# Kernel optimization log

Measured on AMD Instinct MI355X. Metric: run time of the kernel, lower is better.

Reference implementation:

```python
import jax, jax.numpy as jnp
import numpy as np

NHEAD = 16

def setup_inputs() -> dict:
    key = jax.random.key(0)
    ks = jax.random.split(key, 5)
    B, S, D = 4, 2048, 1024
    x = jax.random.normal(ks[0], (B, S, D), dtype=jnp.float32)
    in_proj_weight = jax.random.normal(ks[1], (3 * D, D), dtype=jnp.float32) * (D ** -0.5)
    in_proj_bias = jax.random.normal(ks[2], (3 * D,), dtype=jnp.float32) * 0.02
    out_w = jax.random.normal(ks[3], (D, D), dtype=jnp.float32) * (D ** -0.5)
    out_b = jax.random.normal(ks[4], (D,), dtype=jnp.float32) * 0.02
    return {"x": x, "in_proj_weight": in_proj_weight, "in_proj_bias": in_proj_bias,
            "out_w": out_w, "out_b": out_b}

def reference(x, in_proj_weight, in_proj_bias, out_w, out_b):
    # Faithful to nn.MultiheadAttention self-attn (prefill path, no mask).
    B, S, D = x.shape
    H = NHEAD
    hd = D // H
    qkv = x @ in_proj_weight.T + in_proj_bias            # [B,S,3D]
    q, k, v = jnp.split(qkv, 3, axis=-1)                 # each [B,S,D]
    def heads(t):
        return t.reshape(B, S, H, hd).transpose(0, 2, 1, 3)  # [B,H,S,hd]
    q, k, v = heads(q), heads(k), heads(v)
    scale = hd ** -0.5
    scores = jnp.einsum('bhqd,bhkd->bhqk', q * scale, k)  # [B,H,S,S]
    attn = jax.nn.softmax(scores, axis=-1)
    o = jnp.einsum('bhqk,bhkd->bhqd', attn, v)            # [B,H,S,hd]
    o = o.transpose(0, 2, 1, 3).reshape(B, S, D)
    return o @ out_w.T + out_b
```

## Files before the change

### kernel.cpp

```cpp
#include <hip/hip_runtime.h>
#include <hip/hip_bf16.h>
#include <math.h>

typedef __bf16 bf16_t;
typedef __bf16 bf16x8 __attribute__((ext_vector_type(8)));
typedef float  f32x4  __attribute__((ext_vector_type(4)));

#define DEV __device__ __forceinline__

#define BSZ    4
#define SEQ    2048
#define DMODEL 1024
#define NHEADS 16
#define HDIM   64
#define MROWS  (BSZ*SEQ)
#define KDIM   1024
#define NQKV   (3*DMODEL)

#define GLOAD_LDS16(src, dst)                                                  \
  __builtin_amdgcn_global_load_lds(                                            \
      (__attribute__((address_space(1))) void*)(void*)(src),                   \
      (__attribute__((address_space(3))) void*)(dst), 16, 0, 0)

DEV unsigned cvtpk_bf16(float lo, float hi) {
  unsigned r;
  asm("v_cvt_pk_bf16_f32 %0, %1, %2" : "=v"(r) : "v"(lo), "v"(hi));
  return r;
}

__global__ void cast3_f32_to_bf16(const float* __restrict__ a, int na4,
                                  const float* __restrict__ b, int nb4,
                                  const float* __restrict__ c, int nc4,
                                  bf16_t* __restrict__ oa,
                                  bf16_t* __restrict__ ob,
                                  bf16_t* __restrict__ oc) {
  union U { bf16_t h[4]; uint2 u; };
  int total = na4 + nb4 + nc4;
  for (int i = blockIdx.x * blockDim.x + threadIdx.x; i < total;
       i += gridDim.x * blockDim.x) {
    const float* src; bf16_t* dst; int k;
    if (i < na4)            { src = a; dst = oa; k = i; }
    else if (i < na4 + nb4) { src = b; dst = ob; k = i - na4; }
    else                    { src = c; dst = oc; k = i - na4 - nb4; }
    float4 v = reinterpret_cast<const float4*>(src)[k];
    U r;
    r.h[0] = (bf16_t)v.x; r.h[1] = (bf16_t)v.y;
    r.h[2] = (bf16_t)v.z; r.h[3] = (bf16_t)v.w;
    reinterpret_cast<uint2*>(dst)[k] = r.u;
  }
}

DEV void gemm_tile(const bf16_t* __restrict__ A, const bf16_t* __restrict__ Bt,
                   int row0, int col0, char* smem, f32x4 acc[4][4]) {
  const int t    = threadIdx.x;
  const int lane = t & 63;
  const int wid  = t >> 6;
  const int wm   = (wid >> 1) * 64;
  const int wn   = (wid & 1) * 64;
  const int l15  = lane & 15;
  const int lhi  = lane >> 4;

  char* As = smem;
  char* Bs = smem + 16384;

  const f32x4 fzero = {0.f, 0.f, 0.f, 0.f};
#pragma unroll
  for (int mi = 0; mi < 4; mi++)
#pragma unroll
    for (int ni = 0; ni < 4; ni++) acc[mi][ni] = fzero;

  const char* Abase = (const char*)A;
  const char* Bbase = (const char*)Bt;

  for (int k0 = 0; k0 < KDIM; k0 += 64) {
    __syncthreads();
#pragma unroll
    for (int i = 0; i < 4; i++) {
      int o   = (t + i * 256) * 16;
      int row = o >> 7;
      int cbs = (o & 127) ^ ((row & 7) << 4);
      GLOAD_LDS16(Abase + ((size_t)(row0 + row) * KDIM + k0) * 2 + cbs, As + o);
      GLOAD_LDS16(Bbase + ((size_t)(col0 + row) * KDIM + k0) * 2 + cbs, Bs + o);
    }
    __syncthreads();

#pragma unroll
    for (int ks = 0; ks < 2; ks++) {
      bf16x8 a[4], b[4];
      int byt = ks * 64 + lhi * 16;
#pragma unroll
      for (int mi = 0; mi < 4; mi++) {
        int r = wm + mi * 16 + l15;
        a[mi] = *(const bf16x8*)(As + r * 128 + (byt ^ ((r & 7) << 4)));
      }
#pragma unroll
      for (int ni = 0; ni < 4; ni++) {
        int r = wn + ni * 16 + l15;
        b[ni] = *(const bf16x8*)(Bs + r * 128 + (byt ^ ((r & 7) << 4)));
      }
#pragma unroll
      for (int mi = 0; mi < 4; mi++)
#pragma unroll
        for (int ni = 0; ni < 4; ni++)
          acc[mi][ni] = __builtin_amdgcn_mfma_f32_16x16x32_bf16(
              a[mi], b[ni], acc[mi][ni], 0, 0, 0);
    }
  }
}

__global__ __launch_bounds__(512, 2)
void gemm_qkv_kernel(const bf16_t* __restrict__ xb,
                     const bf16_t* __restrict__ wqkv,
                     const float* __restrict__ bias,
                     bf16_t* __restrict__ Qg, bf16_t* __restrict__ Kg,
                     bf16_t* __restrict__ Vt) {
  __shared__ char smem[147456];

  const int t = threadIdx.x, lane = t & 63, wid = t >> 6;
  const int l15 = lane & 15, lhi = lane >> 4;
  const int wm = (wid >> 2) * 64;
  const int wn = (wid & 3) * 64;

  const int bx = blockIdx.x;
  const int wg = (bx & 7) * 96 + (bx >> 3);
  const int mt = wg / 12, nt = wg % 12;
  const int row0 = mt * 128, col0 = nt * 256;

  const char* Ax = (const char*)xb;
  const char* Bx = (const char*)wqkv;

  auto STAGE8 = [&](int bf, int u) {
    char* Ad = smem + bf * 16384;
    char* Bd = smem + 49152 + bf * 32768;
    size_t kof = (size_t)u * 128;
#pragma unroll
    for (int r = 0; r < 2; r++) {
      int o = (r * 512 + t) * 16;
      int row = o >> 7;
      int cbs = (o & 127) ^ ((row & 7) << 4);
      GLOAD_LDS16(Ax + (((size_t)(row0 + row)) << 11) + kof + cbs, Ad + o);
    }
#pragma unroll
    for (int r = 0; r < 4; r++) {
      int o = (r * 512 + t) * 16;
      int row = o >> 7;
      int cbs = (o & 127) ^ ((row & 7) << 4);
      GLOAD_LDS16(Bx + (((size_t)(col0 + row)) << 11) + kof + cbs, Bd + o);
    }
  };

  f32x4 acc[4][4];
  const f32x4 fzero = {0.f, 0.f, 0.f, 0.f};
#pragma unroll
  for (int mi = 0; mi < 4; mi++)
#pragma unroll
    for (int ni = 0; ni < 4; ni++) acc[mi][ni] = fzero;

  STAGE8(0, 0);
  STAGE8(1, 1);

#pragma unroll
  for (int u = 0; u < 16; u++) {
    if (u < 15) asm volatile("s_waitcnt vmcnt(6)" ::: "memory");
    else        asm volatile("s_waitcnt vmcnt(0)" ::: "memory");
    __builtin_amdgcn_s_barrier();
    if (u + 2 < 16) STAGE8((u + 2) % 3, u + 2);

    char* Ab = smem + (u % 3) * 16384;
    char* Bb = smem + 49152 + (u % 3) * 32768;
#pragma unroll
    for (int ks = 0; ks < 2; ks++) {
      bf16x8 a[4], b[4];
      int byt = ks * 64 + lhi * 16;
#pragma unroll
      for (int mi = 0; mi < 4; mi++) {
        int r = wm + mi * 16 + l15;
        a[mi] = *(const bf16x8*)(Ab + r * 128 + (byt ^ ((r & 7) << 4)));
      }
#pragma unroll
      for (int ni = 0; ni < 4; ni++) {
        int r = wn + ni * 16 + l15;
        b[ni] = *(const bf16x8*)(Bb + r * 128 + (byt ^ ((r & 7) << 4)));
      }
#pragma unroll
      for (int mi = 0; mi < 4; mi++)
#pragma unroll
        for (int ni = 0; ni < 4; ni++)
          acc[mi][ni] = __builtin_amdgcn_mfma_f32_16x16x32_bf16(
              a[mi], b[ni], acc[mi][ni], 0, 0, 0);
    }
  }

  const float qscale = 0.125f * 1.44269504f;

  if (nt < 8) {
#pragma unroll
    for (int mi = 0; mi < 4; mi++)
#pragma unroll
      for (int ni = 0; ni < 4; ni++)
#pragma unroll
        for (int j = 0; j < 4; j++) {
          int m = row0 + wm + mi * 16 + lhi * 4 + j;
          int n = col0 + wn + ni * 16 + l15;
          float v = acc[mi][ni][j] + bias[n];
          int b = m >> 11, s = m & 2047;
          int which = n >> 10, rem = n & 1023;
          int h = rem >> 6, d = rem & 63;
          size_t bh = (size_t)(b * NHEADS + h);
          if (which == 0) {
            Qg[(bh * SEQ + s) * HDIM + d] = (bf16_t)(v * qscale);
          } else {
            Kg[(bh * SEQ + s) * HDIM + d] = (bf16_t)v;
          }
        }
  } else {
    __syncthreads();
#pragma unroll
    for (int mi = 0; mi < 4; mi++)
#pragma unroll
      for (int ni = 0; ni < 4; ni++) {
        int nl = wn + ni * 16 + l15;
        int n  = col0 + nl;
        float bi = bias[n];
        int mbase = wm + mi * 16 + lhi * 4;
        float v0 = acc[mi][ni][0] + bi, v1 = acc[mi][ni][1] + bi;
        float v2 = acc[mi][ni][2] + bi, v3 = acc[mi][ni][3] + bi;
        *(unsigned*)(smem + nl * 272 + mbase * 2)     = cvtpk_bf16(v0, v1);
        *(unsigned*)(smem + nl * 272 + mbase * 2 + 4) = cvtpk_bf16(v2, v3);
      }
    __syncthreads();
    const int b  = row0 >> 11, s0 = row0 & 2047;
    const int hbase = (col0 - 2048) >> 6;
#pragma unroll
    for (int it = 0; it < 8; it++) {
      int idx = it * 512 + t;
      int nl = idx >> 4, T = (idx >> 3) & 1, c = idx & 7;
      const char* rb = smem + nl * 272 + T * 128 + 4 * c;
      unsigned r0 = *(const unsigned*)(rb);
      unsigned r1 = *(const unsigned*)(rb + 32);
      unsigned r2 = *(const unsigned*)(rb + 64);
      unsigned r3 = *(const unsigned*)(rb + 96);
      uint4 o;
      o.x = (r0 & 0xffffu) | (r1 << 16);
      o.y = (r2 & 0xffffu) | (r3 << 16);
      o.z = (r0 >> 16) | (r1 & 0xffff0000u);
      o.w = (r2 >> 16) | (r3 & 0xffff0000u);
      int h = hbase + (nl >> 6), d = nl & 63;
      size_t elem = ((size_t)(b * NHEADS + h) * HDIM + d) * SEQ +
                    (size_t)(s0 + T * 64 + 8 * c);
      *(uint4*)((char*)Vt + elem * 2) = o;
    }
  }
}

__global__ void gemm_out_kernel(const bf16_t* __restrict__ Og,
                                const bf16_t* __restrict__ wo,
                                const float* __restrict__ bias,
                                float* __restrict__ out) {
  __shared__ char smem[32768];
  f32x4 acc[4][4];
  const int bx = blockIdx.x;
  const int wg = (bx & 7) * 64 + (bx >> 3);
  const int mt = wg >> 3, nt = wg & 7;
  const int row0 = mt * 128, col0 = nt * 128;
  gemm_tile(Og, wo, row0, col0, smem, acc);

  const int t = threadIdx.x, lane = t & 63, wid = t >> 6;
  const int wm = (wid >> 1) * 64, wn = (wid & 1) * 64;
  const int l15 = lane & 15, lhi = lane >> 4;
#pragma unroll
  for (int mi = 0; mi < 4; mi++)
#pragma unroll
    for (int ni = 0; ni < 4; ni++)
#pragma unroll
      for (int j = 0; j < 4; j++) {
        int m = row0 + wm + mi * 16 + lhi * 4 + j;
        int n = col0 + wn + ni * 16 + l15;
        out[(size_t)m * DMODEL + n] = acc[mi][ni][j] + bias[n];
      }
}

__global__ __launch_bounds__(512, 2)
void attn_kernel(const bf16_t* __restrict__ Qg,
                 const bf16_t* __restrict__ Kg,
                 const bf16_t* __restrict__ Vt,
                 bf16_t* __restrict__ Og) {
  __shared__ char smem[65536];
  char* Ps = smem + 32768;

  const int t = threadIdx.x, lane = t & 63, w = t >> 6;
  const int l15 = lane & 15, lhi = lane >> 4;
  char* Pw = Ps + w * 4096;

  const int xcd = blockIdx.x & 7, slot = blockIdx.x >> 3;
  const int bh = xcd * 8 + (slot >> 3), qt = slot & 7;

  const char* Kb = (const char*)Kg + (size_t)bh * SEQ * HDIM * 2;
  const char* Vb = (const char*)Vt + (size_t)bh * HDIM * SEQ * 2;

  const int so = t * 16;
  const int srw = so >> 7;
  const int scbs = (so & 127) ^ ((srw & 7) << 4);
  const char* gK = Kb + (size_t)srw * 128 + scbs;
  const char* gV = Vb + (size_t)srw * 4096 + scbs;

  const int swz = (l15 & 7) << 4;
  const int koff0 = l15 * 128 + ((lhi * 16) ^ swz);
  const int koff1 = l15 * 128 + ((64 + lhi * 16) ^ swz);
  int woff[4];
#pragma unroll
  for (int j = 0; j < 4; j++)
    woff[j] = (lhi * 4 + j) * 128 + ((8 * l15) ^ (((lhi * 4 + j) & 7) << 4));

  auto STAGE = [&](int buf, int kt) {
    char* Kd = smem + buf * 16384;
    char* Vd = Kd + 8192;
    GLOAD_LDS16(gK + (size_t)kt * 8192, Kd + so);
    GLOAD_LDS16(gV + (size_t)kt * 128, Vd + so);
  };

  STAGE(1, 0);

  bf16x8 qf[2][2];
#pragma unroll
  for (int mi = 0; mi < 2; mi++)
#pragma unroll
    for (int ks = 0; ks < 2; ks++) {
      int q = qt * 256 + w * 32 + mi * 16 + l15;
      qf[mi][ks] = *(const bf16x8*)((const char*)Qg +
                   ((size_t)bh * SEQ + q) * 128 + ks * 64 + lhi * 16);
    }

  const f32x4 fzero = {0.f, 0.f, 0.f, 0.f};
  float lpart[2][4];
  f32x4 oacc[2][4];
#pragma unroll
  for (int mi = 0; mi < 2; mi++)
#pragma unroll
    for (int j = 0; j < 4; j++) { lpart[mi][j] = 0.f; oacc[mi][j] = fzero; }

  int cur = 1;
  for (int kt = 0; kt < SEQ / 64; kt++) {
    __syncthreads();
    if (kt < SEQ / 64 - 1) STAGE(cur ^ 1, kt + 1);

    char* Ks = smem + cur * 16384;
    char* Vs = Ks + 8192;

    f32x4 sacc[2][4];
#pragma unroll
    for (int mi = 0; mi < 2; mi++)
#pragma unroll
      for (int ni = 0; ni < 4; ni++) sacc[mi][ni] = fzero;
    __builtin_amdgcn_s_setprio(1);
#pragma unroll
    for (int ks = 0; ks < 2; ks++) {
      const int ko = ks ? koff1 : koff0;
      bf16x8 kf[4];
#pragma unroll
      for (int ni = 0; ni < 4; ni++)
        kf[ni] = *(const bf16x8*)(Ks + ko + ni * 2048);
#pragma unroll
      for (int mi = 0; mi < 2; mi++)
#pragma unroll
        for (int ni = 0; ni < 4; ni++)
          sacc[mi][ni] = __builtin_amdgcn_mfma_f32_16x16x32_bf16(
              qf[mi][ks], kf[ni], sacc[mi][ni], 0, 0, 0);
    }
    __builtin_amdgcn_s_setprio(0);

#pragma unroll
    for (int mi = 0; mi < 2; mi++)
#pragma unroll
      for (int j = 0; j < 4; j++) {
        float p[4];
#pragma unroll
        for (int ni = 0; ni < 4; ni++)
          p[ni] = __builtin_amdgcn_exp2f(sacc[mi][ni][j]);
        lpart[mi][j] += (p[0] + p[1]) + (p[2] + p[3]);
        uint2 pk;
        pk.x = cvtpk_bf16(p[0], p[1]);
        pk.y = cvtpk_bf16(p[2], p[3]);
        *(uint2*)(Pw + mi * 2048 + woff[j]) = pk;
      }

    __builtin_amdgcn_s_setprio(1);
#pragma unroll
    for (int ks = 0; ks < 2; ks++) {
      const int ko = ks ? koff1 : koff0;
      bf16x8 pf[2], vf[4];
#pragma unroll
      for (int mi = 0; mi < 2; mi++)
        pf[mi] = *(const bf16x8*)(Pw + ko + mi * 2048);
#pragma unroll
      for (int db = 0; db < 4; db++)
        vf[db] = *(const bf16x8*)(Vs + ko + db * 2048);
#pragma unroll
      for (int mi = 0; mi < 2; mi++)
#pragma unroll
        for (int db = 0; db < 4; db++)
          oacc[mi][db] = __builtin_amdgcn_mfma_f32_16x16x32_bf16(
              pf[mi], vf[db], oacc[mi][db], 0, 0, 0);
    }
    __builtin_amdgcn_s_setprio(0);
    cur ^= 1;
  }

  float linv[2][4];
#pragma unroll
  for (int mi = 0; mi < 2; mi++)
#pragma unroll
    for (int j = 0; j < 4; j++) {
      float ls = lpart[mi][j];
      ls += __shfl_xor(ls, 1, 64);
      ls += __shfl_xor(ls, 2, 64);
      ls += __shfl_xor(ls, 4, 64);
      ls += __shfl_xor(ls, 8, 64);
      linv[mi][j] = 1.0f / ls;
    }
  const int b = bh >> 4, h = bh & 15;
#pragma unroll
  for (int mi = 0; mi < 2; mi++)
#pragma unroll
    for (int db = 0; db < 4; db++)
#pragma unroll
      for (int j = 0; j < 4; j++) {
        int srow = qt * 256 + w * 32 + mi * 16 + lhi * 4 + j;
        int d = db * 16 + l15;
        float v = oacc[mi][db][j] * linv[mi][j];
        Og[((size_t)b * SEQ + srow) * DMODEL + h * HDIM + d] = (bf16_t)v;
      }
}

extern "C" void kernel_launch(void* const* d_in, const int* in_sizes, int n_in,
                              void* d_out, int out_size, void* d_ws,
                              size_t ws_size, hipStream_t stream) {
  (void)in_sizes; (void)n_in; (void)out_size; (void)ws_size;
  const float* x     = (const float*)d_in[0];
  const float* w_in  = (const float*)d_in[1];
  const float* b_in  = (const float*)d_in[2];
  const float* w_out = (const float*)d_in[3];
  const float* b_out = (const float*)d_in[4];
  float* out = (float*)d_out;

  char* ws = (char*)d_ws;
  bf16_t* xb  = (bf16_t*)ws; ws += (size_t)MROWS * KDIM * 2;
  bf16_t* wqb = (bf16_t*)ws; ws += (size_t)NQKV * KDIM * 2;
  bf16_t* wob = (bf16_t*)ws; ws += (size_t)DMODEL * KDIM * 2;
  bf16_t* Qg  = (bf16_t*)ws; ws += (size_t)MROWS * DMODEL * 2;
  bf16_t* Kg  = (bf16_t*)ws; ws += (size_t)MROWS * DMODEL * 2;
  bf16_t* Vt  = (bf16_t*)ws; ws += (size_t)MROWS * DMODEL * 2;
  bf16_t* Og  = (bf16_t*)ws; ws += (size_t)MROWS * DMODEL * 2;

  cast3_f32_to_bf16<<<2048, 256, 0, stream>>>(
      x, MROWS * KDIM / 4, w_in, NQKV * KDIM / 4, w_out, DMODEL * KDIM / 4,
      xb, wqb, wob);

  gemm_qkv_kernel<<<768, 512, 0, stream>>>(xb, wqb, b_in, Qg, Kg, Vt);
  attn_kernel<<<512, 512, 0, stream>>>(Qg, Kg, Vt, Og);
  gemm_out_kernel<<<64 * 8, 256, 0, stream>>>(Og, wob, b_out, out);
}
```

Measured before the change: 159.0 us.

## Rewrite output projection GEMM with triple-buffered async LDS pipeline and larger tiles

```diff
diff --git a/kernel.cpp b/kernel.cpp
--- a/kernel.cpp
+++ b/kernel.cpp
@@ -50,64 +50,6 @@
   }
 }
 
-DEV void gemm_tile(const bf16_t* __restrict__ A, const bf16_t* __restrict__ Bt,
-                   int row0, int col0, char* smem, f32x4 acc[4][4]) {
-  const int t    = threadIdx.x;
-  const int lane = t & 63;
-  const int wid  = t >> 6;
-  const int wm   = (wid >> 1) * 64;
-  const int wn   = (wid & 1) * 64;
-  const int l15  = lane & 15;
-  const int lhi  = lane >> 4;
-
-  char* As = smem;
-  char* Bs = smem + 16384;
-
-  const f32x4 fzero = {0.f, 0.f, 0.f, 0.f};
-#pragma unroll
-  for (int mi = 0; mi < 4; mi++)
-#pragma unroll
-    for (int ni = 0; ni < 4; ni++) acc[mi][ni] = fzero;
-
-  const char* Abase = (const char*)A;
-  const char* Bbase = (const char*)Bt;
-
-  for (int k0 = 0; k0 < KDIM; k0 += 64) {
-    __syncthreads();
-#pragma unroll
-    for (int i = 0; i < 4; i++) {
-      int o   = (t + i * 256) * 16;
-      int row = o >> 7;
-      int cbs = (o & 127) ^ ((row & 7) << 4);
-      GLOAD_LDS16(Abase + ((size_t)(row0 + row) * KDIM + k0) * 2 + cbs, As + o);
-      GLOAD_LDS16(Bbase + ((size_t)(col0 + row) * KDIM + k0) * 2 + cbs, Bs + o);
-    }
-    __syncthreads();
-
-#pragma unroll
-    for (int ks = 0; ks < 2; ks++) {
-      bf16x8 a[4], b[4];
-      int byt = ks * 64 + lhi * 16;
-#pragma unroll
-      for (int mi = 0; mi < 4; mi++) {
-        int r = wm + mi * 16 + l15;
-        a[mi] = *(const bf16x8*)(As + r * 128 + (byt ^ ((r & 7) << 4)));
-      }
-#pragma unroll
-      for (int ni = 0; ni < 4; ni++) {
-        int r = wn + ni * 16 + l15;
-        b[ni] = *(const bf16x8*)(Bs + r * 128 + (byt ^ ((r & 7) << 4)));
-      }
-#pragma unroll
-      for (int mi = 0; mi < 4; mi++)
-#pragma unroll
-        for (int ni = 0; ni < 4; ni++)
-          acc[mi][ni] = __builtin_amdgcn_mfma_f32_16x16x32_bf16(
-              a[mi], b[ni], acc[mi][ni], 0, 0, 0);
-    }
-  }
-}
-
 __global__ __launch_bounds__(512, 2)
 void gemm_qkv_kernel(const bf16_t* __restrict__ xb,
                      const bf16_t* __restrict__ wqkv,
@@ -253,21 +195,88 @@
   }
 }
 
-__global__ void gemm_out_kernel(const bf16_t* __restrict__ Og,
-                                const bf16_t* __restrict__ wo,
-                                const float* __restrict__ bias,
-                                float* __restrict__ out) {
-  __shared__ char smem[32768];
+__global__ __launch_bounds__(512, 2)
+void gemm_out_kernel(const bf16_t* __restrict__ Og,
+                     const bf16_t* __restrict__ wo,
+                     const float* __restrict__ bias,
+                     float* __restrict__ out) {
+  __shared__ char smem[147456];
+
+  const int t = threadIdx.x, lane = t & 63, wid = t >> 6;
+  const int l15 = lane & 15, lhi = lane >> 4;
+  const int wm = (wid >> 2) * 64;
+  const int wn = (wid & 3) * 64;
+
+  const int bx = blockIdx.x;
+  const int wg = (bx & 7) * 32 + (bx >> 3);
+  const int mt = wg >> 2, nt = wg & 3;
+  const int row0 = mt * 128, col0 = nt * 256;
+
+  const char* Ax = (const char*)Og;
+  const char* Bx = (const char*)wo;
+
+  auto STAGE8 = [&](int bf, int u) {
+    char* Ad = smem + bf * 16384;
+    char* Bd = smem + 49152 + bf * 32768;
+    size_t kof = (size_t)u * 128;
+#pragma unroll
+    for (int r = 0; r < 2; r++) {
+      int o = (r * 512 + t) * 16;
+      int row = o >> 7;
+      int cbs = (o & 127) ^ ((row & 7) << 4);
+      GLOAD_LDS16(Ax + (((size_t)(row0 + row)) << 11) + kof + cbs, Ad + o);
+    }
+#pragma unroll
+    for (int r = 0; r < 4; r++) {
+      int o = (r * 512 + t) * 16;
+      int row = o >> 7;
+      int cbs = (o & 127) ^ ((row & 7) << 4);
+      GLOAD_LDS16(Bx + (((size_t)(col0 + row)) << 11) + kof + cbs, Bd + o);
+    }
+  };
+
   f32x4 acc[4][4];
-  const int bx = blockIdx.x;
-  const int wg = (bx & 7) * 64 + (bx >> 3);
-  const int mt = wg >> 3, nt = wg & 7;
-  const int row0 = mt * 128, col0 = nt * 128;
-  gemm_tile(Og, wo, row0, col0, smem, acc);
-
-  const int t = threadIdx.x, lane = t & 63, wid = t >> 6;
-  const int wm = (wid >> 1) * 64, wn = (wid & 1) * 64;
-  const int l15 = lane & 15, lhi = lane >> 4;
+  const f32x4 fzero = {0.f, 0.f, 0.f, 0.f};
+#pragma unroll
+  for (int mi = 0; mi < 4; mi++)
+#pragma unroll
+    for (int ni = 0; ni < 4; ni++) acc[mi][ni] = fzero;
+
+  STAGE8(0, 0);
+  STAGE8(1, 1);
+
+#pragma unroll
+  for (int u = 0; u < 16; u++) {
+    if (u < 15) asm volatile("s_waitcnt vmcnt(6)" ::: "memory");
+    else        asm volatile("s_waitcnt vmcnt(0)" ::: "memory");
+    __builtin_amdgcn_s_barrier();
+    if (u + 2 < 16) STAGE8((u + 2) % 3, u + 2);
+
+    char* Ab = smem + (u % 3) * 16384;
+    char* Bb = smem + 49152 + (u % 3) * 32768;
+#pragma unroll
+    for (int ks = 0; ks < 2; ks++) {
+      bf16x8 a[4], b[4];
+      int byt = ks * 64 + lhi * 16;
+#pragma unroll
+      for (int mi = 0; mi < 4; mi++) {
+        int r = wm + mi * 16 + l15;
+        a[mi] = *(const bf16x8*)(Ab + r * 128 + (byt ^ ((r & 7) << 4)));
+      }
+#pragma unroll
+      for (int ni = 0; ni < 4; ni++) {
+        int r = wn + ni * 16 + l15;
+        b[ni] = *(const bf16x8*)(Bb + r * 128 + (byt ^ ((r & 7) << 4)));
+      }
+#pragma unroll
+      for (int mi = 0; mi < 4; mi++)
+#pragma unroll
+        for (int ni = 0; ni < 4; ni++)
+          acc[mi][ni] = __builtin_amdgcn_mfma_f32_16x16x32_bf16(
+              a[mi], b[ni], acc[mi][ni], 0, 0, 0);
+    }
+  }
+
 #pragma unroll
   for (int mi = 0; mi < 4; mi++)
 #pragma unroll
@@ -458,5 +467,5 @@
 
   gemm_qkv_kernel<<<768, 512, 0, stream>>>(xb, wqb, b_in, Qg, Kg, Vt);
   attn_kernel<<<512, 512, 0, stream>>>(Qg, Kg, Vt, Og);
-  gemm_out_kernel<<<64 * 8, 256, 0, stream>>>(Og, wob, b_out, out);
-}
+  gemm_out_kernel<<<256, 512, 0, stream>>>(Og, wob, b_out, out);
+}
```

Measured after the change: 155.8 us, median of 2. 2.0% less time.
